# Performance work log

Hardware: AMD Instinct MI355X
Metric: run time of the kernel (lower is better)

## Reference

```python
import jax, jax.numpy as jnp
import numpy as np

EMBED_DIM = 1024
HEAD_DIM = 128

def setup_inputs() -> dict:
    key = jax.random.key(0)
    ks = jax.random.split(key, 7)
    B, S = 4, 2048
    x = jax.random.normal(ks[0], (B, S, EMBED_DIM), dtype=jnp.float32)
    # Linear params: weight [embed_dim, head_dim] (applied as x @ W + b), scaled init
    scale = 1.0 / np.sqrt(EMBED_DIM)
    Wq = jax.random.normal(ks[1], (EMBED_DIM, HEAD_DIM), dtype=jnp.float32) * scale
    Wk = jax.random.normal(ks[2], (EMBED_DIM, HEAD_DIM), dtype=jnp.float32) * scale
    Wv = jax.random.normal(ks[3], (EMBED_DIM, HEAD_DIM), dtype=jnp.float32) * scale
    bq = jax.random.normal(ks[4], (HEAD_DIM,), dtype=jnp.float32) * 0.01
    bk = jax.random.normal(ks[5], (HEAD_DIM,), dtype=jnp.float32) * 0.01
    bv = jax.random.normal(ks[6], (HEAD_DIM,), dtype=jnp.float32) * 0.01
    return {"x": x, "Wq": Wq, "bq": bq, "Wk": Wk, "bk": bk, "Wv": Wv, "bv": bv}

def reference(x, Wq, bq, Wk, bk, Wv, bv):
    # x: [B, S, E]
    S = x.shape[1]
    norm = jnp.asarray(HEAD_DIM ** 0.5, x.dtype)
    q = x @ Wq + bq  # [B, S, D]
    k = x @ Wk + bk
    v = x @ Wv + bv
    scores = jnp.einsum('bsd,btd->bst', q, k) / norm  # [B, S, S]
    causal = jnp.tril(jnp.ones((S, S), dtype=bool))
    scores = jnp.where(causal, scores, -jnp.inf)
    att = jax.nn.softmax(scores, axis=-1)
    return jnp.einsum('bst,btd->bsd', att, v)  # [B, S, D]
```

## Files before the change

### kernel.cpp

```cpp
#include <hip/hip_runtime.h>
#include <hip/hip_bf16.h>

typedef __attribute__((ext_vector_type(8))) short short8;
typedef __attribute__((ext_vector_type(4))) float f32x4;

static __device__ __forceinline__ unsigned short f2bf(float f){
  union { float f; unsigned int u; } v; v.f = f;
  unsigned int r = v.u + 0x7fffu + ((v.u >> 16) & 1u);
  return (unsigned short)(r >> 16);
}
static __device__ __forceinline__ float bf2f(unsigned short u){
  union { unsigned int u; float f; } v; v.u = ((unsigned int)u) << 16; return v.f;
}

static __device__ __forceinline__ void load_lds16(const unsigned short* g, unsigned short* l){
  __builtin_amdgcn_global_load_lds(
      (const __attribute__((address_space(1))) unsigned int*)(g),
      (__attribute__((address_space(3))) unsigned int*)(l), 16, 0, 0);
}

__global__ void k_prep(const float* __restrict__ x, unsigned short* __restrict__ xb,
                       const float* __restrict__ Wq, const float* __restrict__ Wk,
                       const float* __restrict__ Wv,
                       const float* __restrict__ bq, const float* __restrict__ bk,
                       const float* __restrict__ bv,
                       unsigned short* __restrict__ Wt, float* __restrict__ bias){
  if (blockIdx.x < 4096){
    int i = (blockIdx.x * 256 + threadIdx.x) * 8;
    float4 a = *(const float4*)(x + i);
    float4 b = *(const float4*)(x + i + 4);
    unsigned short h[8];
    h[0]=f2bf(a.x); h[1]=f2bf(a.y); h[2]=f2bf(a.z); h[3]=f2bf(a.w);
    h[4]=f2bf(b.x); h[5]=f2bf(b.y); h[6]=f2bf(b.z); h[7]=f2bf(b.w);
    *(uint4*)(xb + i) = *(uint4*)h;
  } else {
    int gid = (blockIdx.x - 4096) * 256 + threadIdx.x;
    int p = gid >> 17;
    int rem = gid & 131071;
    int d = rem >> 10, e = rem & 1023;
    const float* W = (p==0) ? Wq : ((p==1) ? Wk : Wv);
    Wt[gid] = f2bf(W[e*128 + d]);
    if (gid < 384){
      int pp = gid >> 7, dd = gid & 127;
      bias[gid] = (pp==0) ? bq[dd] : ((pp==1) ? bk[dd] : bv[dd]);
    }
  }
}

__global__ __launch_bounds__(256) void k_gemm_qkv(
    const unsigned short* __restrict__ Xb, const unsigned short* __restrict__ Wt,
    const float* __restrict__ bias,
    unsigned short* __restrict__ Qsw, unsigned short* __restrict__ Ksw,
    unsigned short* __restrict__ Vsw){
  __shared__ __align__(16) unsigned short As[128*64];
  __shared__ __align__(16) unsigned short Bs[128*64];
  int tid = threadIdx.x;
  int m0 = blockIdx.x * 128;
  int p  = blockIdx.y;
  int w = tid >> 6, lane = tid & 63, quad = lane >> 4, l16 = lane & 15;
  int wm = (w >> 1) * 64, wn = (w & 1) * 64;
  f32x4 acc[4][4];
  #pragma unroll
  for (int i=0;i<4;i++)
    #pragma unroll
    for (int j=0;j<4;j++) acc[i][j] = (f32x4){0.f,0.f,0.f,0.f};

  const unsigned short* Wp = Wt + p * (128*1024);
  int rowbase = w * 32;
  const unsigned short* Ag = Xb + (m0 + rowbase + (lane>>3))*1024 + (lane&7)*8;
  const unsigned short* Bg = Wp + (rowbase + (lane>>3))*1024 + (lane&7)*8;
  unsigned short* Al = As + rowbase*64;
  unsigned short* Bl = Bs + rowbase*64;

  for (int k0 = 0; k0 < 1024; k0 += 64){
    #pragma unroll
    for (int s8=0; s8<4; s8++){
      load_lds16(Ag + k0 + s8*8192, Al + s8*512);
      load_lds16(Bg + k0 + s8*8192, Bl + s8*512);
    }
    __syncthreads();
    #pragma unroll
    for (int kk=0; kk<64; kk+=32){
      short8 af[4], bf[4];
      #pragma unroll
      for (int i=0;i<4;i++) af[i] = *(const short8*)(As + (wm + i*16 + l16)*64 + kk + quad*8);
      #pragma unroll
      for (int j=0;j<4;j++) bf[j] = *(const short8*)(Bs + (wn + j*16 + l16)*64 + kk + quad*8);
      #pragma unroll
      for (int i=0;i<4;i++)
        #pragma unroll
        for (int j=0;j<4;j++)
          acc[i][j] = __builtin_amdgcn_mfma_f32_16x16x32_bf16(af[i], bf[j], acc[i][j], 0,0,0);
    }
    __syncthreads();
  }
  const float qscale = 0.08838834764831845f * 1.44269504088896340f;
  if (p < 2){
    unsigned short* dst = (p==0)? Qsw : Ksw;
    float scale = (p==0)? qscale : 1.0f;
    #pragma unroll
    for (int i=0;i<4;i++){
      #pragma unroll
      for (int j=0;j<4;j++){
        int col = wn + j*16 + l16;
        float bv_ = bias[p*128 + col];
        int kc = col >> 5, q2 = (col >> 3) & 3, jj = col & 7;
        #pragma unroll
        for (int r=0;r<4;r++){
          int row = m0 + wm + i*16 + quad*4 + r;
          int rt = row >> 4, m = row & 15;
          dst[rt*2048 + kc*512 + q2*128 + m*8 + jj] = f2bf((acc[i][j][r] + bv_)*scale);
        }
      }
    }
  } else {
    #pragma unroll
    for (int i=0;i<4;i++){
      int row0 = m0 + wm + i*16 + quad*4;
      int bb = row0 >> 11, s = row0 & 2047;
      int t64 = s >> 6, srem = s & 63;
      int kc2 = srem >> 5, q2v = (srem >> 3) & 3, jjb = srem & 7;
      #pragma unroll
      for (int j=0;j<4;j++){
        int col = wn + j*16 + l16;
        float bv_ = bias[256 + col];
        int nt = (wn + j*16) >> 4;
        unsigned short pk[4];
        #pragma unroll
        for (int r=0;r<4;r++) pk[r] = f2bf(acc[i][j][r] + bv_);
        *(uint2*)(Vsw + (bb*32+t64)*8192 + nt*1024 + kc2*512 + q2v*128 + l16*8 + jjb) = *(uint2*)pk;
      }
    }
  }
}

__global__ __launch_bounds__(64) void k_attn(
    const unsigned short* __restrict__ Qsw, const unsigned short* __restrict__ Ksw,
    const unsigned short* __restrict__ Vsw, unsigned short* __restrict__ Apart){
  __shared__ __align__(16) unsigned short Pw[2*16*80];
  int x = blockIdx.x;
  int b = x & 3;
  int t = x >> 2;
  int c = t & 7;
  int qb = 63 - (t >> 3);
  int T32 = (qb >> 1) + 1;
  int nch = (T32 + 3) >> 2;
  if (c >= nch) return;
  int lane = threadIdx.x;
  int quad = lane >> 4, l16 = lane & 15;
  int q0 = qb * 32;

  short8 aq[2][4];
  #pragma unroll
  for (int s=0;s<2;s++)
    #pragma unroll
    for (int kc=0;kc<4;kc++)
      aq[s][kc] = *(const short8*)(Qsw + (b*128 + qb*2 + s)*2048 + kc*512 + lane*8);

  f32x4 o[2][8];
  #pragma unroll
  for (int s=0;s<2;s++)
    #pragma unroll
    for (int i=0;i<8;i++) o[s][i] = (f32x4){0.f,0.f,0.f,0.f};
  float mcol[2] = {-1e30f,-1e30f};
  float lcol[2] = {0.f,0.f};
  short8 ap[2][2];

  const unsigned short* Kb = Ksw + b*128*2048;
  const unsigned short* Vb = Vsw + b*32*8192;

  int tEnd = (T32 < c*4+4) ? T32 : (c*4+4);
  for (int tt = c*4; tt < tEnd; tt++){
    int t0 = tt * 64;
    f32x4 sc[2][4];
    #pragma unroll
    for (int s=0;s<2;s++)
      #pragma unroll
      for (int nt=0;nt<4;nt++) sc[s][nt] = (f32x4){0.f,0.f,0.f,0.f};
    #pragma unroll
    for (int nt=0;nt<4;nt++){
      const unsigned short* Kt = Kb + ((t0>>4)+nt)*2048 + lane*8;
      #pragma unroll
      for (int kc=0;kc<4;kc++){
        short8 kf = *(const short8*)(Kt + kc*512);
        sc[0][nt] = __builtin_amdgcn_mfma_f32_16x16x32_bf16(kf, aq[0][kc], sc[0][nt], 0,0,0);
        sc[1][nt] = __builtin_amdgcn_mfma_f32_16x16x32_bf16(kf, aq[1][kc], sc[1][nt], 0,0,0);
      }
    }
    #pragma unroll
    for (int s=0;s<2;s++){
      int qs = q0 + s*16;
      if (t0 + 63 > qs){
        #pragma unroll
        for (int nt=0;nt<4;nt++){
          int kb_ = t0 + nt*16 + quad*4;
          #pragma unroll
          for (int r=0;r<4;r++)
            if (kb_ + r > qs + l16) sc[s][nt][r] = -1e30f;
        }
      }
      float mt_ = -1e30f;
      #pragma unroll
      for (int nt=0;nt<4;nt++)
        #pragma unroll
        for (int r=0;r<4;r++) mt_ = fmaxf(mt_, sc[s][nt][r]);
      mt_ = fmaxf(mt_, __shfl_xor(mt_, 16));
      mt_ = fmaxf(mt_, __shfl_xor(mt_, 32));
      float mn = fmaxf(mcol[s], mt_);
      float al = exp2f(mcol[s] - mn);
      mcol[s] = mn;
      float ls = 0.f;
      #pragma unroll
      for (int nt=0;nt<4;nt++)
        #pragma unroll
        for (int r=0;r<4;r++){
          float pv = exp2f(sc[s][nt][r] - mn);
          sc[s][nt][r] = pv;
          ls += pv;
        }
      ls += __shfl_xor(ls, 16);
      ls += __shfl_xor(ls, 32);
      lcol[s] = lcol[s]*al + ls;
      #pragma unroll
      for (int r=0;r<4;r++){
        float ar = __shfl(al, quad*4 + r);
        #pragma unroll
        for (int nt=0;nt<8;nt++) o[s][nt][r] *= ar;
      }
      unsigned short* Pws = Pw + s*1280;
      #pragma unroll
      for (int nt=0;nt<4;nt++){
        unsigned short pk[4];
        #pragma unroll
        for (int r=0;r<4;r++) pk[r] = f2bf(sc[s][nt][r]);
        *(uint2*)(Pws + l16*80 + nt*16 + quad*4) = *(uint2*)pk;
      }
      ap[s][0] = *(const short8*)(Pws + l16*80 + quad*8);
      ap[s][1] = *(const short8*)(Pws + l16*80 + 32 + quad*8);
    }
    const unsigned short* Vt0 = Vb + (t0>>6)*8192 + lane*8;
    #pragma unroll
    for (int nt=0; nt<8; nt++)
      #pragma unroll
      for (int kc2=0;kc2<2;kc2++){
        short8 vf = *(const short8*)(Vt0 + nt*1024 + kc2*512);
        o[0][nt] = __builtin_amdgcn_mfma_f32_16x16x32_bf16(ap[0][kc2], vf, o[0][nt], 0,0,0);
        o[1][nt] = __builtin_amdgcn_mfma_f32_16x16x32_bf16(ap[1][kc2], vf, o[1][nt], 0,0,0);
      }
  }

  unsigned short* slot = Apart + (size_t)(((b*64 + qb)*8 + c)) * 4224;
  #pragma unroll
  for (int s=0;s<2;s++)
    #pragma unroll
    for (int nt=0;nt<8;nt++){
      unsigned short pk[4];
      #pragma unroll
      for (int r=0;r<4;r++) pk[r] = f2bf(o[s][nt][r]);
      *(uint2*)(slot + (s*8+nt)*256 + lane*4) = *(uint2*)pk;
    }
  float* fslot = (float*)(slot + 4096);
  if (quad == 0){
    #pragma unroll
    for (int s=0;s<2;s++){
      fslot[s*16 + l16]      = mcol[s];
      fslot[32 + s*16 + l16] = lcol[s];
    }
  }
}

__global__ __launch_bounds__(256) void k_acomb(const unsigned short* __restrict__ Apart,
                                               float* __restrict__ out){
  int b = blockIdx.x & 3, qb = blockIdx.x >> 2;
  int T32 = (qb >> 1) + 1;
  int nch = (T32 + 3) >> 2;
  const unsigned short* slot0 = Apart + (size_t)((b*64 + qb)*8) * 4224;
  int tid = threadIdx.x;
  int row = tid >> 3;
  int c0 = (tid & 7) * 16;
  int s = row >> 4, qrow = row & 15;
  int quad = qrow >> 2, r = qrow & 3;
  int nt = c0 >> 4;
  float m = -1e30f;
  for (int c=0;c<nch;c++){
    const float* fs = (const float*)(slot0 + c*4224 + 4096);
    m = fmaxf(m, fs[s*16 + qrow]);
  }
  float acc[16];
  #pragma unroll
  for (int k=0;k<16;k++) acc[k] = 0.f;
  float lsum = 0.f;
  for (int c=0;c<nch;c++){
    const float* fs = (const float*)(slot0 + c*4224 + 4096);
    float e = exp2f(fs[s*16 + qrow] - m);
    lsum += fs[32 + s*16 + qrow] * e;
    const unsigned short* ob = slot0 + c*4224 + (s*8+nt)*256 + quad*64 + r;
    #pragma unroll
    for (int k=0;k<16;k++)
      acc[k] += bf2f(ob[k*4]) * e;
  }
  float inv = 1.0f / lsum;
  float* op = out + (size_t)(b*2048 + qb*32 + row)*128 + c0;
  #pragma unroll
  for (int g=0;g<4;g++){
    float4 rv = {acc[g*4]*inv, acc[g*4+1]*inv, acc[g*4+2]*inv, acc[g*4+3]*inv};
    *(float4*)(op + g*4) = rv;
  }
}

extern "C" void kernel_launch(void* const* d_in, const int* in_sizes, int n_in,
                              void* d_out, int out_size, void* d_ws, size_t ws_size,
                              hipStream_t stream) {
  const float* x  = (const float*)d_in[0];
  const float* Wq = (const float*)d_in[1];
  const float* bq = (const float*)d_in[2];
  const float* Wk = (const float*)d_in[3];
  const float* bk = (const float*)d_in[4];
  const float* Wv = (const float*)d_in[5];
  const float* bv = (const float*)d_in[6];
  char* ws = (char*)d_ws;
  unsigned short* Xb   = (unsigned short*)(ws);
  unsigned short* Wt   = (unsigned short*)(ws + 16777216);
  float*          bias = (float*)(ws + 17563648);
  unsigned short* Qsw  = (unsigned short*)(ws + 17565184);
  unsigned short* Ksw  = (unsigned short*)(ws + 19662336);
  unsigned short* Vsw  = (unsigned short*)(ws + 21759488);
  unsigned short* Apart= (unsigned short*)(ws + 23856640);
  float* out = (float*)d_out;

  hipLaunchKernelGGL(k_prep,    dim3(5632),  dim3(256), 0, stream, x, Xb, Wq, Wk, Wv, bq, bk, bv, Wt, bias);
  hipLaunchKernelGGL(k_gemm_qkv,dim3(64,3),  dim3(256), 0, stream, Xb, Wt, bias, Qsw, Ksw, Vsw);
  hipLaunchKernelGGL(k_attn,    dim3(2048),  dim3(64),  0, stream, Qsw, Ksw, Vsw, Apart);
  hipLaunchKernelGGL(k_acomb,   dim3(256),   dim3(256), 0, stream, Apart, out);
}
```

Before: 144.1 us.

## Fuse split-KV combine into attention via last-block atomic counter; LDS-transpose weights

Drops the separate combine kernel. Each attention block now atomically bumps a per-(batch, query-block) counter, and the last chunk to finish merges all partial outputs with an online-softmax rescale and writes the final fp32 result. The weight transpose in the prep kernel now goes through a padded LDS tile, so both global reads and writes are coalesced, and that kernel also zeroes the counters. This removes one launch and the strided transpose reads, at the cost of thread fences, atomics, and a serial combine tail in one 64-thread block.

```diff
diff --git a/kernel.cpp b/kernel.cpp
--- a/kernel.cpp
+++ b/kernel.cpp
@@ -24,26 +24,40 @@
                        const float* __restrict__ Wv,
                        const float* __restrict__ bq, const float* __restrict__ bk,
                        const float* __restrict__ bv,
-                       unsigned short* __restrict__ Wt, float* __restrict__ bias){
-  if (blockIdx.x < 4096){
-    int i = (blockIdx.x * 256 + threadIdx.x) * 8;
+                       unsigned short* __restrict__ Wt, float* __restrict__ bias,
+                       unsigned int* __restrict__ cnt){
+  int bx = blockIdx.x, tid = threadIdx.x;
+  if (bx < 4096){
+    int i = (bx * 256 + tid) * 8;
     float4 a = *(const float4*)(x + i);
     float4 b = *(const float4*)(x + i + 4);
     unsigned short h[8];
     h[0]=f2bf(a.x); h[1]=f2bf(a.y); h[2]=f2bf(a.z); h[3]=f2bf(a.w);
     h[4]=f2bf(b.x); h[5]=f2bf(b.y); h[6]=f2bf(b.z); h[7]=f2bf(b.w);
     *(uint4*)(xb + i) = *(uint4*)h;
-  } else {
-    int gid = (blockIdx.x - 4096) * 256 + threadIdx.x;
-    int p = gid >> 17;
-    int rem = gid & 131071;
-    int d = rem >> 10, e = rem & 1023;
-    const float* W = (p==0) ? Wq : ((p==1) ? Wk : Wv);
-    Wt[gid] = f2bf(W[e*128 + d]);
-    if (gid < 384){
-      int pp = gid >> 7, dd = gid & 127;
-      bias[gid] = (pp==0) ? bq[dd] : ((pp==1) ? bk[dd] : bv[dd]);
-    }
+    return;
+  }
+  __shared__ float Lt[64*129];
+  int w0 = bx - 4096;
+  int p = w0 >> 4, e0 = (w0 & 15) * 64;
+  const float* W = (p==0) ? Wq : ((p==1) ? Wk : Wv);
+  #pragma unroll
+  for (int it=0; it<32; it++){
+    int idx = it*256 + tid;
+    int e = idx >> 7, d = idx & 127;
+    Lt[e*129 + d] = W[(e0 + e)*128 + d];
+  }
+  if (w0 == 0){
+    bias[tid] = (tid < 128) ? bq[tid] : bk[tid - 128];
+    if (tid < 128) bias[256 + tid] = bv[tid];
+  }
+  if (w0 == 1) cnt[tid] = 0;
+  __syncthreads();
+  #pragma unroll
+  for (int it=0; it<32; it++){
+    int idx = it*256 + tid;
+    int d = idx >> 6, e = idx & 63;
+    Wt[p*131072 + d*1024 + e0 + e] = f2bf(Lt[e*129 + d]);
   }
 }
 
@@ -136,7 +150,8 @@
 
 __global__ __launch_bounds__(64) void k_attn(
     const unsigned short* __restrict__ Qsw, const unsigned short* __restrict__ Ksw,
-    const unsigned short* __restrict__ Vsw, unsigned short* __restrict__ Apart){
+    const unsigned short* __restrict__ Vsw, unsigned short* __restrict__ Apart,
+    unsigned int* __restrict__ cnt, float* __restrict__ out){
   __shared__ __align__(16) unsigned short Pw[2*16*80];
   int x = blockIdx.x;
   int b = x & 3;
@@ -267,45 +282,66 @@
       fslot[32 + s*16 + l16] = lcol[s];
     }
   }
-}
-
-__global__ __launch_bounds__(256) void k_acomb(const unsigned short* __restrict__ Apart,
-                                               float* __restrict__ out){
-  int b = blockIdx.x & 3, qb = blockIdx.x >> 2;
-  int T32 = (qb >> 1) + 1;
-  int nch = (T32 + 3) >> 2;
-  const unsigned short* slot0 = Apart + (size_t)((b*64 + qb)*8) * 4224;
-  int tid = threadIdx.x;
-  int row = tid >> 3;
-  int c0 = (tid & 7) * 16;
-  int s = row >> 4, qrow = row & 15;
-  int quad = qrow >> 2, r = qrow & 3;
-  int nt = c0 >> 4;
-  float m = -1e30f;
-  for (int c=0;c<nch;c++){
-    const float* fs = (const float*)(slot0 + c*4224 + 4096);
-    m = fmaxf(m, fs[s*16 + qrow]);
-  }
-  float acc[16];
-  #pragma unroll
-  for (int k=0;k<16;k++) acc[k] = 0.f;
-  float lsum = 0.f;
-  for (int c=0;c<nch;c++){
-    const float* fs = (const float*)(slot0 + c*4224 + 4096);
-    float e = exp2f(fs[s*16 + qrow] - m);
-    lsum += fs[32 + s*16 + qrow] * e;
-    const unsigned short* ob = slot0 + c*4224 + (s*8+nt)*256 + quad*64 + r;
-    #pragma unroll
-    for (int k=0;k<16;k++)
-      acc[k] += bf2f(ob[k*4]) * e;
-  }
-  float inv = 1.0f / lsum;
-  float* op = out + (size_t)(b*2048 + qb*32 + row)*128 + c0;
-  #pragma unroll
-  for (int g=0;g<4;g++){
-    float4 rv = {acc[g*4]*inv, acc[g*4+1]*inv, acc[g*4+2]*inv, acc[g*4+3]*inv};
-    *(float4*)(op + g*4) = rv;
-  }
+
+  __threadfence();
+  unsigned int old = 0;
+  if (lane == 0) old = atomicAdd(&cnt[b*64 + qb], 1u);
+  old = (unsigned int)__shfl((int)old, 0);
+  if (old != (unsigned int)(nch - 1)) return;
+  __threadfence();
+
+  const unsigned short* base = Apart + (size_t)((b*64 + qb)*8) * 4224;
+  float m_[2][4], lsm[2][4], acc[2][8][4];
+  #pragma unroll
+  for (int s=0;s<2;s++)
+    #pragma unroll
+    for (int r=0;r<4;r++){ m_[s][r] = -1e30f; lsm[s][r] = 0.f; }
+  #pragma unroll
+  for (int s=0;s<2;s++)
+    #pragma unroll
+    for (int nt=0;nt<8;nt++)
+      #pragma unroll
+      for (int r=0;r<4;r++) acc[s][nt][r] = 0.f;
+
+  for (int cc=0; cc<nch; cc++){
+    const float* fs = (const float*)(base + cc*4224 + 4096);
+    float ec[2][4];
+    #pragma unroll
+    for (int s=0;s<2;s++)
+      #pragma unroll
+      for (int r=0;r<4;r++){
+        float mc = fs[s*16 + quad*4 + r];
+        float lc = fs[32 + s*16 + quad*4 + r];
+        float nm = fmaxf(m_[s][r], mc);
+        float eo = exp2f(m_[s][r] - nm);
+        ec[s][r] = exp2f(mc - nm);
+        m_[s][r] = nm;
+        lsm[s][r] = lsm[s][r]*eo + lc*ec[s][r];
+        #pragma unroll
+        for (int nt=0;nt<8;nt++) acc[s][nt][r] *= eo;
+      }
+    #pragma unroll
+    for (int s=0;s<2;s++)
+      #pragma unroll
+      for (int nt=0;nt<8;nt++){
+        uint2 raw = *(const uint2*)(base + cc*4224 + (s*8+nt)*256 + lane*4);
+        const unsigned short* pr = (const unsigned short*)&raw;
+        #pragma unroll
+        for (int r=0;r<4;r++) acc[s][nt][r] += bf2f(pr[r]) * ec[s][r];
+      }
+  }
+  float inv[2][4];
+  #pragma unroll
+  for (int s=0;s<2;s++)
+    #pragma unroll
+    for (int r=0;r<4;r++) inv[s][r] = 1.0f / lsm[s][r];
+  #pragma unroll
+  for (int s=0;s<2;s++)
+    #pragma unroll
+    for (int nt=0;nt<8;nt++)
+      #pragma unroll
+      for (int r=0;r<4;r++)
+        out[(size_t)(b*2048 + q0 + s*16 + quad*4 + r)*128 + nt*16 + l16] = acc[s][nt][r] * inv[s][r];
 }
 
 extern "C" void kernel_launch(void* const* d_in, const int* in_sizes, int n_in,
@@ -326,10 +362,11 @@
   unsigned short* Ksw  = (unsigned short*)(ws + 19662336);
   unsigned short* Vsw  = (unsigned short*)(ws + 21759488);
   unsigned short* Apart= (unsigned short*)(ws + 23856640);
+  unsigned int*   cnt  = (unsigned int*)(ws + 41158144);
   float* out = (float*)d_out;
 
-  hipLaunchKernelGGL(k_prep,    dim3(5632),  dim3(256), 0, stream, x, Xb, Wq, Wk, Wv, bq, bk, bv, Wt, bias);
+  hipLaunchKernelGGL(k_prep,    dim3(4144),  dim3(256), 0, stream,
+                     x, Xb, Wq, Wk, Wv, bq, bk, bv, Wt, bias, cnt);
   hipLaunchKernelGGL(k_gemm_qkv,dim3(64,3),  dim3(256), 0, stream, Xb, Wt, bias, Qsw, Ksw, Vsw);
-  hipLaunchKernelGGL(k_attn,    dim3(2048),  dim3(64),  0, stream, Qsw, Ksw, Vsw, Apart);
-  hipLaunchKernelGGL(k_acomb,   dim3(256),   dim3(256), 0, stream, Apart, out);
-}
+  hipLaunchKernelGGL(k_attn,    dim3(2048),  dim3(64),  0, stream, Qsw, Ksw, Vsw, Apart, cnt, out);
+}
```

Result: slower. 178.2 us (+23.6%).

## Split QKV GEMM along K, add combine kernel, halve attention chunk size

Applied to the files above, without the earlier changes.

The QKV projection GEMM now splits the K dimension in two, raising the grid from 192 to 384 blocks. Each block writes fp32 partial tiles to workspace, and a new k_gcomb kernel sums them, adds the bias, scales and writes the swizzled Q/K/V. The weight transpose in k_prep now goes through an LDS tile so both reads and writes are coalesced. Attention chunks drop from 4 to 2 key tiles, doubling the number of attention blocks (16 chunk slots per query block) to improve load balance. The cost is an extra kernel launch, about 25MB of extra fp32 partial traffic, and more partials for k_acomb to merge.

```diff
diff --git a/kernel.cpp b/kernel.cpp
--- a/kernel.cpp
+++ b/kernel.cpp
@@ -25,38 +25,49 @@
                        const float* __restrict__ bq, const float* __restrict__ bk,
                        const float* __restrict__ bv,
                        unsigned short* __restrict__ Wt, float* __restrict__ bias){
-  if (blockIdx.x < 4096){
-    int i = (blockIdx.x * 256 + threadIdx.x) * 8;
+  int bx = blockIdx.x, tid = threadIdx.x;
+  if (bx < 4096){
+    int i = (bx * 256 + tid) * 8;
     float4 a = *(const float4*)(x + i);
     float4 b = *(const float4*)(x + i + 4);
     unsigned short h[8];
     h[0]=f2bf(a.x); h[1]=f2bf(a.y); h[2]=f2bf(a.z); h[3]=f2bf(a.w);
     h[4]=f2bf(b.x); h[5]=f2bf(b.y); h[6]=f2bf(b.z); h[7]=f2bf(b.w);
     *(uint4*)(xb + i) = *(uint4*)h;
-  } else {
-    int gid = (blockIdx.x - 4096) * 256 + threadIdx.x;
-    int p = gid >> 17;
-    int rem = gid & 131071;
-    int d = rem >> 10, e = rem & 1023;
-    const float* W = (p==0) ? Wq : ((p==1) ? Wk : Wv);
-    Wt[gid] = f2bf(W[e*128 + d]);
-    if (gid < 384){
-      int pp = gid >> 7, dd = gid & 127;
-      bias[gid] = (pp==0) ? bq[dd] : ((pp==1) ? bk[dd] : bv[dd]);
-    }
+    return;
+  }
+  __shared__ float Lt[64*129];
+  int w0 = bx - 4096;
+  int p = w0 >> 4, e0 = (w0 & 15) * 64;
+  const float* W = (p==0) ? Wq : ((p==1) ? Wk : Wv);
+  #pragma unroll
+  for (int it=0; it<32; it++){
+    int idx = it*256 + tid;
+    int e = idx >> 7, d = idx & 127;
+    Lt[e*129 + d] = W[(e0 + e)*128 + d];
+  }
+  if (w0 == 0){
+    bias[tid] = (tid < 128) ? bq[tid] : bk[tid - 128];
+    if (tid < 128) bias[256 + tid] = bv[tid];
+  }
+  __syncthreads();
+  #pragma unroll
+  for (int it=0; it<32; it++){
+    int idx = it*256 + tid;
+    int d = idx >> 6, e = idx & 63;
+    Wt[p*131072 + d*1024 + e0 + e] = f2bf(Lt[e*129 + d]);
   }
 }
 
 __global__ __launch_bounds__(256) void k_gemm_qkv(
     const unsigned short* __restrict__ Xb, const unsigned short* __restrict__ Wt,
-    const float* __restrict__ bias,
-    unsigned short* __restrict__ Qsw, unsigned short* __restrict__ Ksw,
-    unsigned short* __restrict__ Vsw){
+    float* __restrict__ Cp){
   __shared__ __align__(16) unsigned short As[128*64];
   __shared__ __align__(16) unsigned short Bs[128*64];
   int tid = threadIdx.x;
   int m0 = blockIdx.x * 128;
   int p  = blockIdx.y;
+  int kh = blockIdx.z;
   int w = tid >> 6, lane = tid & 63, quad = lane >> 4, l16 = lane & 15;
   int wm = (w >> 1) * 64, wn = (w & 1) * 64;
   f32x4 acc[4][4];
@@ -72,7 +83,8 @@
   unsigned short* Al = As + rowbase*64;
   unsigned short* Bl = Bs + rowbase*64;
 
-  for (int k0 = 0; k0 < 1024; k0 += 64){
+  int kbeg = kh*512, kend = kbeg + 512;
+  for (int k0 = kbeg; k0 < kend; k0 += 64){
     #pragma unroll
     for (int s8=0; s8<4; s8++){
       load_lds16(Ag + k0 + s8*8192, Al + s8*512);
@@ -94,42 +106,59 @@
     }
     __syncthreads();
   }
+  float* slot = Cp + (size_t)(((p*64 + blockIdx.x)*2 + kh)) * 16384;
+  #pragma unroll
+  for (int i=0;i<4;i++)
+    #pragma unroll
+    for (int j=0;j<4;j++)
+      #pragma unroll
+      for (int r=0;r<4;r++)
+        slot[(wm + i*16 + quad*4 + r)*128 + wn + j*16 + l16] = acc[i][j][r];
+}
+
+__global__ __launch_bounds__(256) void k_gcomb(const float* __restrict__ Cp,
+    const float* __restrict__ bias,
+    unsigned short* __restrict__ Qsw, unsigned short* __restrict__ Ksw,
+    unsigned short* __restrict__ Vsw){
+  int mt = blockIdx.x, p = blockIdx.y, tid = threadIdx.x;
+  const float* c0p = Cp + (size_t)((p*64+mt)*2) * 16384;
+  const float* c1p = c0p + 16384;
+  int m0 = mt*128;
   const float qscale = 0.08838834764831845f * 1.44269504088896340f;
   if (p < 2){
     unsigned short* dst = (p==0)? Qsw : Ksw;
     float scale = (p==0)? qscale : 1.0f;
-    #pragma unroll
-    for (int i=0;i<4;i++){
-      #pragma unroll
-      for (int j=0;j<4;j++){
-        int col = wn + j*16 + l16;
-        float bv_ = bias[p*128 + col];
-        int kc = col >> 5, q2 = (col >> 3) & 3, jj = col & 7;
-        #pragma unroll
-        for (int r=0;r<4;r++){
-          int row = m0 + wm + i*16 + quad*4 + r;
-          int rt = row >> 4, m = row & 15;
-          dst[rt*2048 + kc*512 + q2*128 + m*8 + jj] = f2bf((acc[i][j][r] + bv_)*scale);
-        }
-      }
+    for (int it=0; it<16; it++){
+      int g = it*256 + tid;
+      int row = g >> 5, cs = (g & 31)*4;
+      f32x4 a = *(const f32x4*)(c0p + row*128 + cs);
+      f32x4 bb = *(const f32x4*)(c1p + row*128 + cs);
+      int grow = m0 + row;
+      int rt = grow >> 4, m = grow & 15;
+      int kc = cs >> 5, q2 = (cs >> 3) & 3, jj = cs & 7;
+      unsigned short pk[4];
+      #pragma unroll
+      for (int k=0;k<4;k++) pk[k] = f2bf((a[k]+bb[k]+bias[p*128+cs+k])*scale);
+      *(uint2*)(dst + rt*2048 + kc*512 + q2*128 + m*8 + jj) = *(uint2*)pk;
     }
   } else {
-    #pragma unroll
-    for (int i=0;i<4;i++){
-      int row0 = m0 + wm + i*16 + quad*4;
-      int bb = row0 >> 11, s = row0 & 2047;
+    for (int it=0; it<16; it++){
+      int g = it*256 + tid;
+      int col = g & 127, rg = g >> 7;
+      int r0 = rg*4;
+      float bv_ = bias[256 + col];
+      unsigned short pk[4];
+      #pragma unroll
+      for (int k=0;k<4;k++){
+        int row = r0 + k;
+        pk[k] = f2bf(c0p[row*128+col] + c1p[row*128+col] + bv_);
+      }
+      int grow0 = m0 + r0;
+      int bb2 = grow0 >> 11, s = grow0 & 2047;
       int t64 = s >> 6, srem = s & 63;
-      int kc2 = srem >> 5, q2v = (srem >> 3) & 3, jjb = srem & 7;
-      #pragma unroll
-      for (int j=0;j<4;j++){
-        int col = wn + j*16 + l16;
-        float bv_ = bias[256 + col];
-        int nt = (wn + j*16) >> 4;
-        unsigned short pk[4];
-        #pragma unroll
-        for (int r=0;r<4;r++) pk[r] = f2bf(acc[i][j][r] + bv_);
-        *(uint2*)(Vsw + (bb*32+t64)*8192 + nt*1024 + kc2*512 + q2v*128 + l16*8 + jjb) = *(uint2*)pk;
-      }
+      int kc2 = srem >> 5, q2 = (srem >> 3) & 3, jj = srem & 7;
+      int nt = col >> 4, l2 = col & 15;
+      *(uint2*)(Vsw + (bb2*32+t64)*8192 + nt*1024 + kc2*512 + q2*128 + l2*8 + jj) = *(uint2*)pk;
     }
   }
 }
@@ -141,10 +170,10 @@
   int x = blockIdx.x;
   int b = x & 3;
   int t = x >> 2;
-  int c = t & 7;
-  int qb = 63 - (t >> 3);
+  int c = t & 15;
+  int qb = 63 - (t >> 4);
   int T32 = (qb >> 1) + 1;
-  int nch = (T32 + 3) >> 2;
+  int nch = (T32 + 1) >> 1;
   if (c >= nch) return;
   int lane = threadIdx.x;
   int quad = lane >> 4, l16 = lane & 15;
@@ -169,8 +198,8 @@
   const unsigned short* Kb = Ksw + b*128*2048;
   const unsigned short* Vb = Vsw + b*32*8192;
 
-  int tEnd = (T32 < c*4+4) ? T32 : (c*4+4);
-  for (int tt = c*4; tt < tEnd; tt++){
+  int tEnd = (T32 < c*2+2) ? T32 : (c*2+2);
+  for (int tt = c*2; tt < tEnd; tt++){
     int t0 = tt * 64;
     f32x4 sc[2][4];
     #pragma unroll
@@ -249,7 +278,7 @@
       }
   }
 
-  unsigned short* slot = Apart + (size_t)(((b*64 + qb)*8 + c)) * 4224;
+  unsigned short* slot = Apart + (size_t)(((b*64 + qb)*16 + c)) * 4224;
   #pragma unroll
   for (int s=0;s<2;s++)
     #pragma unroll
@@ -273,8 +302,8 @@
                                                float* __restrict__ out){
   int b = blockIdx.x & 3, qb = blockIdx.x >> 2;
   int T32 = (qb >> 1) + 1;
-  int nch = (T32 + 3) >> 2;
-  const unsigned short* slot0 = Apart + (size_t)((b*64 + qb)*8) * 4224;
+  int nch = (T32 + 1) >> 1;
+  const unsigned short* slot0 = Apart + (size_t)((b*64 + qb)*16) * 4224;
   int tid = threadIdx.x;
   int row = tid >> 3;
   int c0 = (tid & 7) * 16;
@@ -325,11 +354,14 @@
   unsigned short* Qsw  = (unsigned short*)(ws + 17565184);
   unsigned short* Ksw  = (unsigned short*)(ws + 19662336);
   unsigned short* Vsw  = (unsigned short*)(ws + 21759488);
-  unsigned short* Apart= (unsigned short*)(ws + 23856640);
+  float*          Cp   = (float*)(ws + 23856640);
+  unsigned short* Apart= (unsigned short*)(ws + 49022464);
   float* out = (float*)d_out;
 
-  hipLaunchKernelGGL(k_prep,    dim3(5632),  dim3(256), 0, stream, x, Xb, Wq, Wk, Wv, bq, bk, bv, Wt, bias);
-  hipLaunchKernelGGL(k_gemm_qkv,dim3(64,3),  dim3(256), 0, stream, Xb, Wt, bias, Qsw, Ksw, Vsw);
-  hipLaunchKernelGGL(k_attn,    dim3(2048),  dim3(64),  0, stream, Qsw, Ksw, Vsw, Apart);
-  hipLaunchKernelGGL(k_acomb,   dim3(256),   dim3(256), 0, stream, Apart, out);
-}
+  hipLaunchKernelGGL(k_prep,    dim3(4144),   dim3(256), 0, stream,
+                     x, Xb, Wq, Wk, Wv, bq, bk, bv, Wt, bias);
+  hipLaunchKernelGGL(k_gemm_qkv,dim3(64,3,2), dim3(256), 0, stream, Xb, Wt, Cp);
+  hipLaunchKernelGGL(k_gcomb,   dim3(64,3),   dim3(256), 0, stream, Cp, bias, Qsw, Ksw, Vsw);
+  hipLaunchKernelGGL(k_attn,    dim3(4096),   dim3(64),  0, stream, Qsw, Ksw, Vsw, Apart);
+  hipLaunchKernelGGL(k_acomb,   dim3(256),    dim3(256), 0, stream, Apart, out);
+}
```

Result: slower. 148.9 us (+3.3%).

## Split-K the QKV GEMM across two blocks and transpose weights via LDS

Applied to the files above, without the earlier changes.

The QKV projection GEMM now splits the K dimension in half, launching a grid of 64x3x2 (384 blocks) instead of 192 so more CUs on the device are occupied. Each half writes fp32 partials to a workspace, and an atomic counter picks the second finisher to add the peer partial and run the bias, scale and swizzled store epilogue. The weight transpose in the prep kernel is rewritten to stage tiles in padded shared memory, so global reads and writes are coalesced, and it also zeroes the counters. The cost is extra fp32 partial traffic (about 25 MB written plus half of that read back), threadfence and atomic synchronisation, and a larger workspace.

```diff
diff --git a/kernel.cpp b/kernel.cpp
--- a/kernel.cpp
+++ b/kernel.cpp
@@ -24,32 +24,47 @@
                        const float* __restrict__ Wv,
                        const float* __restrict__ bq, const float* __restrict__ bk,
                        const float* __restrict__ bv,
-                       unsigned short* __restrict__ Wt, float* __restrict__ bias){
-  if (blockIdx.x < 4096){
-    int i = (blockIdx.x * 256 + threadIdx.x) * 8;
+                       unsigned short* __restrict__ Wt, float* __restrict__ bias,
+                       unsigned int* __restrict__ cnt){
+  int bx = blockIdx.x, tid = threadIdx.x;
+  if (bx < 4096){
+    int i = (bx * 256 + tid) * 8;
     float4 a = *(const float4*)(x + i);
     float4 b = *(const float4*)(x + i + 4);
     unsigned short h[8];
     h[0]=f2bf(a.x); h[1]=f2bf(a.y); h[2]=f2bf(a.z); h[3]=f2bf(a.w);
     h[4]=f2bf(b.x); h[5]=f2bf(b.y); h[6]=f2bf(b.z); h[7]=f2bf(b.w);
     *(uint4*)(xb + i) = *(uint4*)h;
-  } else {
-    int gid = (blockIdx.x - 4096) * 256 + threadIdx.x;
-    int p = gid >> 17;
-    int rem = gid & 131071;
-    int d = rem >> 10, e = rem & 1023;
-    const float* W = (p==0) ? Wq : ((p==1) ? Wk : Wv);
-    Wt[gid] = f2bf(W[e*128 + d]);
-    if (gid < 384){
-      int pp = gid >> 7, dd = gid & 127;
-      bias[gid] = (pp==0) ? bq[dd] : ((pp==1) ? bk[dd] : bv[dd]);
-    }
+    return;
+  }
+  __shared__ float Lt[64*129];
+  int w0 = bx - 4096;
+  int p = w0 >> 4, e0 = (w0 & 15) * 64;
+  const float* W = (p==0) ? Wq : ((p==1) ? Wk : Wv);
+  #pragma unroll
+  for (int it=0; it<32; it++){
+    int idx = it*256 + tid;
+    int e = idx >> 7, d = idx & 127;
+    Lt[e*129 + d] = W[(e0 + e)*128 + d];
+  }
+  if (w0 == 0){
+    bias[tid] = (tid < 128) ? bq[tid] : bk[tid - 128];
+    if (tid < 128) bias[256 + tid] = bv[tid];
+  }
+  if (w0 == 1 && tid < 192) cnt[tid] = 0;
+  __syncthreads();
+  #pragma unroll
+  for (int it=0; it<32; it++){
+    int idx = it*256 + tid;
+    int d = idx >> 6, e = idx & 63;
+    Wt[p*131072 + d*1024 + e0 + e] = f2bf(Lt[e*129 + d]);
   }
 }
 
 __global__ __launch_bounds__(256) void k_gemm_qkv(
     const unsigned short* __restrict__ Xb, const unsigned short* __restrict__ Wt,
-    const float* __restrict__ bias,
+    const float* __restrict__ bias, float* __restrict__ Cp,
+    unsigned int* __restrict__ cnt,
     unsigned short* __restrict__ Qsw, unsigned short* __restrict__ Ksw,
     unsigned short* __restrict__ Vsw){
   __shared__ __align__(16) unsigned short As[128*64];
@@ -57,6 +72,7 @@
   int tid = threadIdx.x;
   int m0 = blockIdx.x * 128;
   int p  = blockIdx.y;
+  int kh = blockIdx.z;
   int w = tid >> 6, lane = tid & 63, quad = lane >> 4, l16 = lane & 15;
   int wm = (w >> 1) * 64, wn = (w & 1) * 64;
   f32x4 acc[4][4];
@@ -72,7 +88,8 @@
   unsigned short* Al = As + rowbase*64;
   unsigned short* Bl = Bs + rowbase*64;
 
-  for (int k0 = 0; k0 < 1024; k0 += 64){
+  int kbeg = kh*512, kend = kbeg + 512;
+  for (int k0 = kbeg; k0 < kend; k0 += 64){
     #pragma unroll
     for (int s8=0; s8<4; s8++){
       load_lds16(Ag + k0 + s8*8192, Al + s8*512);
@@ -94,6 +111,33 @@
     }
     __syncthreads();
   }
+
+  int pair = p*64 + blockIdx.x;
+  float* slot = Cp + (size_t)(pair*2 + kh) * 16384;
+  #pragma unroll
+  for (int i=0;i<4;i++)
+    #pragma unroll
+    for (int j=0;j<4;j++)
+      #pragma unroll
+      for (int r=0;r<4;r++)
+        slot[(wm + i*16 + quad*4 + r)*128 + wn + j*16 + l16] = acc[i][j][r];
+
+  __threadfence();
+  __shared__ unsigned int s_old;
+  if (tid == 0) s_old = atomicAdd(&cnt[pair], 1u);
+  __syncthreads();
+  if (s_old == 0) return;
+  __threadfence();
+
+  const float* peer = Cp + (size_t)(pair*2 + (1-kh)) * 16384;
+  #pragma unroll
+  for (int i=0;i<4;i++)
+    #pragma unroll
+    for (int j=0;j<4;j++)
+      #pragma unroll
+      for (int r=0;r<4;r++)
+        acc[i][j][r] += peer[(wm + i*16 + quad*4 + r)*128 + wn + j*16 + l16];
+
   const float qscale = 0.08838834764831845f * 1.44269504088896340f;
   if (p < 2){
     unsigned short* dst = (p==0)? Qsw : Ksw;
@@ -325,11 +369,15 @@
   unsigned short* Qsw  = (unsigned short*)(ws + 17565184);
   unsigned short* Ksw  = (unsigned short*)(ws + 19662336);
   unsigned short* Vsw  = (unsigned short*)(ws + 21759488);
-  unsigned short* Apart= (unsigned short*)(ws + 23856640);
+  float*          Cp   = (float*)(ws + 23856640);
+  unsigned int*   cnt  = (unsigned int*)(ws + 49022464);
+  unsigned short* Apart= (unsigned short*)(ws + 49026560);
   float* out = (float*)d_out;
 
-  hipLaunchKernelGGL(k_prep,    dim3(5632),  dim3(256), 0, stream, x, Xb, Wq, Wk, Wv, bq, bk, bv, Wt, bias);
-  hipLaunchKernelGGL(k_gemm_qkv,dim3(64,3),  dim3(256), 0, stream, Xb, Wt, bias, Qsw, Ksw, Vsw);
-  hipLaunchKernelGGL(k_attn,    dim3(2048),  dim3(64),  0, stream, Qsw, Ksw, Vsw, Apart);
-  hipLaunchKernelGGL(k_acomb,   dim3(256),   dim3(256), 0, stream, Apart, out);
-}
+  hipLaunchKernelGGL(k_prep,    dim3(4144),   dim3(256), 0, stream,
+                     x, Xb, Wq, Wk, Wv, bq, bk, bv, Wt, bias, cnt);
+  hipLaunchKernelGGL(k_gemm_qkv,dim3(64,3,2), dim3(256), 0, stream,
+                     Xb, Wt, bias, Cp, cnt, Qsw, Ksw, Vsw);
+  hipLaunchKernelGGL(k_attn,    dim3(2048),   dim3(64),  0, stream, Qsw, Ksw, Vsw, Apart);
+  hipLaunchKernelGGL(k_acomb,   dim3(256),    dim3(256), 0, stream, Apart, out);
+}
```

After: 206.4 us. 1.43x slower.
